# Kernel optimization log

Hardware: AMD Instinct MI355X
Metric: run time of the kernel (lower is better)

## Reference

```python
import jax, jax.numpy as jnp
import numpy as np

N = 50000          # nodes
E = 1_600_000      # edges (avg degree 32)
IN_N, IN_E = 16, 1 # fc_encoder hardwired input dims
H = 128            # per-layer out_node/out_edge channels (out//2 = 64 inner)
BN_EPS = 1e-5


def setup_inputs() -> dict:
    key = jax.random.key(0)
    ks = jax.random.split(key, 32)
    d = {}
    d["x"] = jax.random.normal(ks[0], (N, IN_N), jnp.float32)
    d["edge_attr"] = jax.random.normal(ks[1], (E, IN_E), jnp.float32)
    d["edge_index"] = jax.random.randint(ks[2], (2, E), 0, N)
    i = 3
    for l, (ni, ei) in enumerate([(IN_N, IN_E), (H, H)]):
        s_n = 1.0 / np.sqrt(ni)
        s_e = 1.0 / np.sqrt(ei)
        s_h = 1.0 / np.sqrt(H)
        d[f"l{l}_Wn"] = jax.random.normal(ks[i], (H // 2, ni), jnp.float32) * s_n; i += 1
        d[f"l{l}_We"] = jax.random.normal(ks[i], (H // 2, ei), jnp.float32) * s_e; i += 1
        d[f"l{l}_Wfn"] = jax.random.normal(ks[i], (H, H), jnp.float32) * s_h; i += 1
        d[f"l{l}_bfn"] = jax.random.normal(ks[i], (H,), jnp.float32) * s_h; i += 1
        d[f"l{l}_Wfe"] = jax.random.normal(ks[i], (H, H), jnp.float32) * s_h; i += 1
        d[f"l{l}_bfe"] = jax.random.normal(ks[i], (H,), jnp.float32) * s_h; i += 1
        d[f"l{l}_g"] = jax.random.uniform(ks[i], (H,), jnp.float32, 0.5, 1.5); i += 1
        d[f"l{l}_b"] = jax.random.normal(ks[i], (H,), jnp.float32) * 0.1; i += 1
        d[f"l{l}_rm"] = jax.random.normal(ks[i], (H,), jnp.float32) * 0.1; i += 1
        d[f"l{l}_rv"] = jax.random.uniform(ks[i], (H,), jnp.float32, 0.5, 1.5); i += 1
    return d


def _layer(x, ea, src, dst, Wn, We, Wfn, bfn, Wfe, bfe, g, b, rm, rv):
    # NodeEdgeInteraction_node (eval mode: dropout = identity)
    n1 = jax.nn.relu(x @ Wn.T)            # [N, H/2]
    e1 = jax.nn.relu(ea @ We.T)           # [E, H/2]
    # edge_updater: cat([n1[src] + n1[dst], e1])
    e2 = jnp.concatenate([n1[src] + n1[dst], e1], axis=-1)      # [E, H]
    # propagate: message = e1, sum-aggregate at destination (edge_index[1])
    agg = jax.ops.segment_sum(e1, dst, num_segments=x.shape[0])  # [N, H/2]
    n2 = jnp.concatenate([agg, n1], axis=-1)                     # [N, H]
    n2 = jax.nn.relu(n2 @ Wfn.T + bfn)
    e2 = jax.nn.relu(e2 @ Wfe.T + bfe)
    # BatchNorm1d (eval: running stats)
    n2 = (n2 - rm) * jax.lax.rsqrt(rv + BN_EPS) * g + b
    return n2, e2


def reference(x, edge_attr, edge_index,
              l0_Wn, l0_We, l0_Wfn, l0_bfn, l0_Wfe, l0_bfe, l0_g, l0_b, l0_rm, l0_rv,
              l1_Wn, l1_We, l1_Wfn, l1_bfn, l1_Wfe, l1_bfe, l1_g, l1_b, l1_rm, l1_rv):
    src, dst = edge_index[0], edge_index[1]
    x, edge_attr = _layer(x, edge_attr, src, dst,
                          l0_Wn, l0_We, l0_Wfn, l0_bfn, l0_Wfe, l0_bfe,
                          l0_g, l0_b, l0_rm, l0_rv)
    x, edge_attr = _layer(x, edge_attr, src, dst,
                          l1_Wn, l1_We, l1_Wfn, l1_bfn, l1_Wfe, l1_bfe,
                          l1_g, l1_b, l1_rm, l1_rv)
    return x  # GNNEncoder returns node embeddings only
```

## Files before the change

kernel.cpp:

```cpp
#include <hip/hip_runtime.h>

typedef unsigned short u16;
typedef __attribute__((ext_vector_type(8))) short short8;
typedef __attribute__((ext_vector_type(4))) float floatx4;

#define NN 50000
#define NE 1600000
#define BN_EPS 1e-5f
#define TPB 8

#define LDS_BARRIER() asm volatile("s_waitcnt lgkmcnt(0)\n\ts_barrier" ::: "memory")

__device__ __forceinline__ float bfu(u16 u) {
    union { unsigned u32; float f; } v; v.u32 = ((unsigned)u) << 16; return v.f;
}
__device__ __forceinline__ u16 f2bf(float f) {
    union { float f; unsigned u; } v; v.f = f;
    unsigned r = v.u + 0x7FFFu + ((v.u >> 16) & 1u);
    return (u16)(r >> 16);
}
__device__ __forceinline__ float ldf(const void* p, int i, int m) {
    return m ? ((const float*)p)[i] : bfu(((const u16*)p)[i]);
}

__global__ __launch_bounds__(256) void k_cvtw(const u16* __restrict__ x,
                                              const void* __restrict__ W0, const void* __restrict__ W1,
                                              const void* __restrict__ W2, const void* __restrict__ W3,
                                              const void* __restrict__ W4,
                                              const void* __restrict__ We0raw,
                                              u16* __restrict__ dst, float* __restrict__ PN,
                                              int* __restrict__ mode) {
    int t = threadIdx.x;
    __shared__ float sred[4];
    float mx = 0.f;
    for (int i = t; i < 4096; i += 256) mx = fmaxf(mx, fabsf(bfu(x[i])));
#pragma unroll
    for (int o = 32; o > 0; o >>= 1) mx = fmaxf(mx, __shfl_down(mx, o));
    if ((t & 63) == 0) sred[t >> 6] = mx;
    __syncthreads();
    float m2 = fmaxf(fmaxf(sred[0], sred[1]), fmaxf(sred[2], sred[3]));
    int m = (m2 > 1e4f) ? 1 : 0;
    if (blockIdx.x == 0 && t == 0) mode[0] = m;
    if (blockIdx.x == 256) {
        if (t < 128) {
            float p = 0.f, n = 0.f;
            for (int k = 0; k < 64; k++) {
                float w = ldf(We0raw, k, m);
                float wf = ldf(W0, t * 128 + 64 + k, m);
                p += fmaxf(w, 0.f) * wf;
                n += fminf(w, 0.f) * wf;
            }
            PN[t] = p; PN[128 + t] = n;
        }
        return;
    }
    int i = blockIdx.x * 256 + t;
    const void* src; int off;
    if (i < 16384)      { src = W0; off = i; }
    else if (i < 24576) { src = W1; off = i - 16384; }
    else if (i < 40960) { src = W2; off = i - 24576; }
    else if (i < 49152) { src = W3; off = i - 40960; }
    else                { src = W4; off = i - 49152; }
    dst[i] = m ? f2bf(((const float*)src)[off]) : ((const u16*)src)[off];
}

__global__ __launch_bounds__(256) void k_enc0h(const void* __restrict__ x, const void* __restrict__ Wn,
                                               u16* __restrict__ n1, const int* __restrict__ ei,
                                               const void* __restrict__ ea,
                                               float* __restrict__ sp, float* __restrict__ sn,
                                               const int* __restrict__ mf) {
    int b = blockIdx.x;
    int t = threadIdx.x;
    int m = mf[0];
    if (b >= 3125) {
        int e = (b - 3125) * 256 + t;
        float a = ldf(ea, e, m);
        int d = ei[NE + e];
        if (a > 0.f) atomicAdd(sp + d, a);
        else if (a < 0.f) atomicAdd(sn + d, a);
        return;
    }
    __shared__ float Wns[64 * 17];
    __shared__ float xsh[16][17];
    int n0 = b * 16;
    for (int i = t; i < 1024; i += 256) Wns[(i >> 4) * 17 + (i & 15)] = ldf(Wn, i, m);
    xsh[t >> 4][t & 15] = ldf(x, n0 * 16 + t, m);
    __syncthreads();
    int c = t & 63, ng = t >> 6;
    float a0 = 0.f, a1 = 0.f, a2 = 0.f, a3 = 0.f;
#pragma unroll
    for (int k = 0; k < 16; k++) {
        float wv = Wns[c * 17 + k];
        a0 += xsh[ng * 4 + 0][k] * wv;
        a1 += xsh[ng * 4 + 1][k] * wv;
        a2 += xsh[ng * 4 + 2][k] * wv;
        a3 += xsh[ng * 4 + 3][k] * wv;
    }
    n1[(n0 + ng * 4 + 0) * 64 + c] = f2bf(fmaxf(a0, 0.f));
    n1[(n0 + ng * 4 + 1) * 64 + c] = f2bf(fmaxf(a1, 0.f));
    n1[(n0 + ng * 4 + 2) * 64 + c] = f2bf(fmaxf(a2, 0.f));
    n1[(n0 + ng * 4 + 3) * 64 + c] = f2bf(fmaxf(a3, 0.f));
}

__global__ __launch_bounds__(256) void k_z(const u16* __restrict__ n1l0, const u16* __restrict__ Wfe0c,
                                           const void* __restrict__ bfe0, u16* __restrict__ z,
                                           const int* __restrict__ mf) {
    int m = mf[0];
    __shared__ __align__(16) u16 fs[64][72];
    int t = threadIdx.x;
    int n0 = blockIdx.x * 64;
    {
        int col = t & 63, rb = t >> 6;
#pragma unroll
        for (int i = 0; i < 16; i++) {
            int row = rb * 16 + i;
            int n = n0 + row;
            fs[row][col] = (n < NN) ? n1l0[n * 64 + col] : (u16)0;
        }
    }
    __syncthreads();
    int lane = t & 63, w = t >> 6, q = lane >> 4, nidx = lane & 15;
    const u16* ar = &fs[w * 16 + nidx][0];
    short8 a0 = *(const short8*)&ar[q * 8];
    short8 a1 = *(const short8*)&ar[32 + q * 8];
#pragma unroll
    for (int jt = 0; jt < 8; jt++) {
        int j = jt * 16 + nidx;
        const u16* wr = Wfe0c + j * 128;
        floatx4 acc = {0.f, 0.f, 0.f, 0.f};
        acc = __builtin_amdgcn_mfma_f32_16x16x32_bf16(a0, *(const short8*)&wr[q * 8], acc, 0, 0, 0);
        acc = __builtin_amdgcn_mfma_f32_16x16x32_bf16(a1, *(const short8*)&wr[32 + q * 8], acc, 0, 0, 0);
        float hb = 0.5f * ldf(bfe0, j, m);
#pragma unroll
        for (int r = 0; r < 4; r++) {
            int row = w * 16 + q * 4 + r;
            int n = n0 + row;
            if (n < NN) z[(size_t)n * 128 + j] = f2bf(acc[r] + hb);
        }
    }
}

__global__ __launch_bounds__(256) void k_node_l0(
    const u16* __restrict__ n1l0, const float* __restrict__ sp, const float* __restrict__ sn,
    const void* __restrict__ We0, const u16* __restrict__ Wfn0c, const void* __restrict__ bfn0,
    const void* __restrict__ g0, const void* __restrict__ b0,
    const void* __restrict__ rm0, const void* __restrict__ rv0,
    const u16* __restrict__ Wn1c, u16* __restrict__ n1l1, const int* __restrict__ mf) {
    int m = mf[0];
    __shared__ __align__(16) u16 fs[64][136];
    __shared__ __align__(16) u16 xs[64][136];
    int t = threadIdx.x;
    int n0 = blockIdx.x * 64;
    {
        int col = t & 127;
        int rbase = t >> 7;
        float wp = 0.f, wn = 0.f;
        if (col < 64) { float w0 = ldf(We0, col, m); wp = fmaxf(w0, 0.f); wn = fminf(w0, 0.f); }
#pragma unroll
        for (int i = 0; i < 32; i++) {
            int row = rbase + 2 * i;
            int n = n0 + row;
            float v = 0.f;
            if (n < NN) v = (col < 64) ? (wp * sp[n] + wn * sn[n]) : bfu(n1l0[n * 64 + col - 64]);
            fs[row][col] = f2bf(v);
        }
    }
    __syncthreads();
    int lane = t & 63, w = t >> 6, q = lane >> 4, nidx = lane & 15;
    {
        const u16* ar = &fs[w * 16 + nidx][0];
        short8 a0 = *(const short8*)&ar[q * 8];
        short8 a1 = *(const short8*)&ar[32 + q * 8];
        short8 a2 = *(const short8*)&ar[64 + q * 8];
        short8 a3 = *(const short8*)&ar[96 + q * 8];
#pragma unroll
        for (int jt = 0; jt < 8; jt++) {
            int j = jt * 16 + nidx;
            const u16* wr = Wfn0c + j * 128;
            floatx4 acc = {0.f, 0.f, 0.f, 0.f};
            acc = __builtin_amdgcn_mfma_f32_16x16x32_bf16(a0, *(const short8*)&wr[q * 8], acc, 0, 0, 0);
            acc = __builtin_amdgcn_mfma_f32_16x16x32_bf16(a1, *(const short8*)&wr[32 + q * 8], acc, 0, 0, 0);
            acc = __builtin_amdgcn_mfma_f32_16x16x32_bf16(a2, *(const short8*)&wr[64 + q * 8], acc, 0, 0, 0);
            acc = __builtin_amdgcn_mfma_f32_16x16x32_bf16(a3, *(const short8*)&wr[96 + q * 8], acc, 0, 0, 0);
            float bias = ldf(bfn0, j, m);
            float sc = ldf(g0, j, m) * rsqrtf(ldf(rv0, j, m) + BN_EPS);
            float sh = ldf(b0, j, m) - ldf(rm0, j, m) * sc;
#pragma unroll
            for (int r = 0; r < 4; r++) {
                int row = w * 16 + q * 4 + r;
                xs[row][j] = f2bf(fmaxf(acc[r] + bias, 0.f) * sc + sh);
            }
        }
    }
    __syncthreads();
    {
        const u16* ar = &xs[w * 16 + nidx][0];
        short8 a0 = *(const short8*)&ar[q * 8];
        short8 a1 = *(const short8*)&ar[32 + q * 8];
        short8 a2 = *(const short8*)&ar[64 + q * 8];
        short8 a3 = *(const short8*)&ar[96 + q * 8];
#pragma unroll
        for (int jt = 0; jt < 4; jt++) {
            int j = jt * 16 + nidx;
            const u16* wr = Wn1c + j * 128;
            floatx4 acc = {0.f, 0.f, 0.f, 0.f};
            acc = __builtin_amdgcn_mfma_f32_16x16x32_bf16(a0, *(const short8*)&wr[q * 8], acc, 0, 0, 0);
            acc = __builtin_amdgcn_mfma_f32_16x16x32_bf16(a1, *(const short8*)&wr[32 + q * 8], acc, 0, 0, 0);
            acc = __builtin_amdgcn_mfma_f32_16x16x32_bf16(a2, *(const short8*)&wr[64 + q * 8], acc, 0, 0, 0);
            acc = __builtin_amdgcn_mfma_f32_16x16x32_bf16(a3, *(const short8*)&wr[96 + q * 8], acc, 0, 0, 0);
#pragma unroll
            for (int r = 0; r < 4; r++) {
                int row = w * 16 + q * 4 + r;
                int n = n0 + row;
                if (n < NN) n1l1[n * 64 + j] = f2bf(fmaxf(acc[r], 0.f));
            }
        }
    }
}

__global__ __launch_bounds__(256) void k_edge9(
    const int* __restrict__ ei, const void* __restrict__ ea, const u16* __restrict__ z,
    const float* __restrict__ PN, const u16* __restrict__ We1c,
    float* __restrict__ agg, const int* __restrict__ mf) {
    int m = mf[0];
    __shared__ __align__(16) u16 h1s[2][16][136];
    int t = threadIdx.x;
    int lane = t & 63, w = t >> 6, q = lane >> 4, nidx = lane & 15;
    int ko = w * 32 + q * 8;
    float Pk[8], Nk[8];
#pragma unroll
    for (int j = 0; j < 8; j++) { Pk[j] = PN[ko + j]; Nk[j] = PN[128 + ko + j]; }
    int c2 = w * 16 + nidx;
    const u16* wr2 = We1c + c2 * 128;
    short8 wB0 = *(const short8*)&wr2[q * 8];
    short8 wB1 = *(const short8*)&wr2[32 + q * 8];
    short8 wB2 = *(const short8*)&wr2[64 + q * 8];
    short8 wB3 = *(const short8*)&wr2[96 + q * 8];

    int e0 = blockIdx.x * (16 * TPB);
    unsigned pk[TPB];
    float av[TPB];
#pragma unroll
    for (int tl = 0; tl < TPB; tl++) {
        int en = e0 + tl * 16 + nidx;
        unsigned s = (unsigned)ei[en];
        unsigned d = (unsigned)ei[NE + en];
        pk[tl] = s | (d << 16);
        av[tl] = ldf(ea, en, m);
    }
    short8 zsb[2], zdb[2];
#pragma unroll
    for (int tl = 0; tl < 2; tl++) {
        unsigned s = pk[tl] & 0xFFFFu, d = pk[tl] >> 16;
        zsb[tl] = *(const short8*)&z[(size_t)s * 128 + ko];
        zdb[tl] = *(const short8*)&z[(size_t)d * 128 + ko];
    }

#pragma unroll
    for (int tile = 0; tile < TPB; tile++) {
        short8 czs = zsb[tile & 1], czd = zdb[tile & 1];
        if (tile + 2 < TPB) {
            unsigned s = pk[tile + 2] & 0xFFFFu, d = pk[tile + 2] >> 16;
            zsb[tile & 1] = *(const short8*)&z[(size_t)s * 128 + ko];
            zdb[tile & 1] = *(const short8*)&z[(size_t)d * 128 + ko];
        }
        float cura = av[tile];
        float pf = fmaxf(cura, 0.f), nf = fminf(cura, 0.f);
        short8 hp;
#pragma unroll
        for (int j = 0; j < 8; j++) {
            float v = bfu((u16)czs[j]) + bfu((u16)czd[j]) + pf * Pk[j] + nf * Nk[j];
            hp[j] = (short)f2bf(fmaxf(v, 0.f));
        }
        *(short8*)&h1s[tile & 1][nidx][ko] = hp;
        LDS_BARRIER();
        const u16* arow = &h1s[tile & 1][nidx][0];
        floatx4 accA = {0.f, 0.f, 0.f, 0.f};
        floatx4 accB = {0.f, 0.f, 0.f, 0.f};
        accA = __builtin_amdgcn_mfma_f32_16x16x32_bf16(*(const short8*)&arow[q * 8], wB0, accA, 0, 0, 0);
        accB = __builtin_amdgcn_mfma_f32_16x16x32_bf16(*(const short8*)&arow[32 + q * 8], wB1, accB, 0, 0, 0);
        accA = __builtin_amdgcn_mfma_f32_16x16x32_bf16(*(const short8*)&arow[64 + q * 8], wB2, accA, 0, 0, 0);
        accB = __builtin_amdgcn_mfma_f32_16x16x32_bf16(*(const short8*)&arow[96 + q * 8], wB3, accB, 0, 0, 0);
        int pkt = (int)pk[tile];
        unsigned x0 = (unsigned)__shfl(pkt, q * 4 + 0);
        unsigned x1 = (unsigned)__shfl(pkt, q * 4 + 1);
        unsigned x2 = (unsigned)__shfl(pkt, q * 4 + 2);
        unsigned x3 = (unsigned)__shfl(pkt, q * 4 + 3);
        atomicAdd(agg + (size_t)(x0 >> 16) * 64 + c2, fmaxf(accA[0] + accB[0], 0.f));
        atomicAdd(agg + (size_t)(x1 >> 16) * 64 + c2, fmaxf(accA[1] + accB[1], 0.f));
        atomicAdd(agg + (size_t)(x2 >> 16) * 64 + c2, fmaxf(accA[2] + accB[2], 0.f));
        atomicAdd(agg + (size_t)(x3 >> 16) * 64 + c2, fmaxf(accA[3] + accB[3], 0.f));
    }
}

__global__ __launch_bounds__(256) void k_node_l1(
    const u16* __restrict__ n1l1, const float* __restrict__ agg,
    const u16* __restrict__ Wfn1c, const void* __restrict__ bfn1,
    const void* __restrict__ g1, const void* __restrict__ b1,
    const void* __restrict__ rm1, const void* __restrict__ rv1,
    void* __restrict__ out, const int* __restrict__ mf) {
    int m = mf[0];
    __shared__ __align__(16) u16 fs[64][136];
    int t = threadIdx.x;
    int n0 = blockIdx.x * 64;
    {
        int col = t & 127;
        int rbase = t >> 7;
#pragma unroll
        for (int i = 0; i < 32; i++) {
            int row = rbase + 2 * i;
            int n = n0 + row;
            float v = 0.f;
            if (n < NN) v = (col < 64) ? agg[n * 64 + col] : bfu(n1l1[n * 64 + col - 64]);
            fs[row][col] = f2bf(v);
        }
    }
    __syncthreads();
    int lane = t & 63, w = t >> 6, q = lane >> 4, nidx = lane & 15;
    const u16* ar = &fs[w * 16 + nidx][0];
    short8 a0 = *(const short8*)&ar[q * 8];
    short8 a1 = *(const short8*)&ar[32 + q * 8];
    short8 a2 = *(const short8*)&ar[64 + q * 8];
    short8 a3 = *(const short8*)&ar[96 + q * 8];
#pragma unroll
    for (int jt = 0; jt < 8; jt++) {
        int j = jt * 16 + nidx;
        const u16* wr = Wfn1c + j * 128;
        floatx4 acc = {0.f, 0.f, 0.f, 0.f};
        acc = __builtin_amdgcn_mfma_f32_16x16x32_bf16(a0, *(const short8*)&wr[q * 8], acc, 0, 0, 0);
        acc = __builtin_amdgcn_mfma_f32_16x16x32_bf16(a1, *(const short8*)&wr[32 + q * 8], acc, 0, 0, 0);
        acc = __builtin_amdgcn_mfma_f32_16x16x32_bf16(a2, *(const short8*)&wr[64 + q * 8], acc, 0, 0, 0);
        acc = __builtin_amdgcn_mfma_f32_16x16x32_bf16(a3, *(const short8*)&wr[96 + q * 8], acc, 0, 0, 0);
        float bias = ldf(bfn1, j, m);
        float sc = ldf(g1, j, m) * rsqrtf(ldf(rv1, j, m) + BN_EPS);
        float sh = ldf(b1, j, m) - ldf(rm1, j, m) * sc;
#pragma unroll
        for (int r = 0; r < 4; r++) {
            int row = w * 16 + q * 4 + r;
            int n = n0 + row;
            if (n < NN) {
                float v = fmaxf(acc[r] + bias, 0.f) * sc + sh;
                if (m) ((float*)out)[n * 128 + j] = v;
                else   ((u16*)out)[n * 128 + j] = f2bf(v);
            }
        }
    }
}

extern "C" void kernel_launch(void* const* d_in, const int* in_sizes, int n_in,
                              void* d_out, int out_size, void* d_ws, size_t ws_size,
                              hipStream_t stream) {
    const void* x    = d_in[0];
    const void* ea   = d_in[1];
    const int*  ei   = (const int*)d_in[2];
    const void* Wn0  = d_in[3];
    const void* We0  = d_in[4];
    const void* Wfn0 = d_in[5];
    const void* bfn0 = d_in[6];
    const void* Wfe0 = d_in[7];
    const void* bfe0 = d_in[8];
    const void* g0   = d_in[9];
    const void* b0   = d_in[10];
    const void* rm0  = d_in[11];
    const void* rv0  = d_in[12];
    const void* Wn1  = d_in[13];
    const void* We1  = d_in[14];
    const void* Wfn1 = d_in[15];
    const void* bfn1 = d_in[16];
    const void* g1   = d_in[19];
    const void* b1   = d_in[20];
    const void* rm1  = d_in[21];
    const void* rv1  = d_in[22];

    float* wsf    = (float*)d_ws;
    float* agg    = wsf;
    u16*   n1l0   = (u16*)(wsf + 3200000);
    u16*   n1l1   = (u16*)(wsf + 4800000);
    float* sp     = wsf + 6400000;
    float* sn     = wsf + 6450000;
    float* PN     = wsf + 6500000;
    u16*   Wc     = (u16*)(wsf + 6500256);
    int*   mode   = (int*)(wsf + 6533024);
    u16*   z      = (u16*)(wsf + 6533028);
    u16* Wfe0c = Wc;
    u16* We1c  = Wc + 16384;
    u16* Wfn0c = Wc + 24576;
    u16* Wn1c  = Wc + 40960;
    u16* Wfn1c = Wc + 49152;

    hipMemsetAsync(sp, 0, 100000 * sizeof(float), stream);
    hipMemsetAsync(agg, 0, 3200000 * sizeof(float), stream);

    k_cvtw<<<257, 256, 0, stream>>>((const u16*)x, Wfe0, We1, Wfn0, Wn1, Wfn1,
                                    We0, Wc, PN, mode);
    k_enc0h<<<9375, 256, 0, stream>>>(x, Wn0, n1l0, ei, ea, sp, sn, mode);
    k_z<<<782, 256, 0, stream>>>(n1l0, Wfe0c, bfe0, z, mode);
    k_node_l0<<<782, 256, 0, stream>>>(n1l0, sp, sn, We0, Wfn0c, bfn0,
                                       g0, b0, rm0, rv0, Wn1c, n1l1, mode);
    k_edge9<<<NE / (16 * TPB), 256, 0, stream>>>(ei, ea, z, PN, We1c, agg, mode);
    k_node_l1<<<782, 256, 0, stream>>>(n1l1, agg, Wfn1c, bfn1,
                                       g1, b1, rm1, rv1, d_out, mode);
}
```

Measured before the change: 620.1 us.

## Sort edges by destination and combine atomics per run in edge kernel

Adds a counting sort of edges by destination: per-node counts, a three-kernel prefix scan, and a scatter that writes packed src/dst pairs and edge attributes into a scratch area in the output buffer. The edge kernel then reads the sorted edges and accumulates consecutive same-destination rows in registers, issuing one atomic per run instead of one per edge. This targets the cost of float atomics into agg. In exchange it adds four small kernels, an atomic-based scatter that reads and writes 1.6M edges, and the output buffer is reused as temporary storage before the final kernel writes it.

```diff
diff --git a/kernel.cpp b/kernel.cpp
--- a/kernel.cpp
+++ b/kernel.cpp
@@ -7,6 +7,7 @@
 #define NN 50000
 #define NE 1600000
 #define BN_EPS 1e-5f
+#define NSCAN 196
 #define TPB 8
 
 #define LDS_BARRIER() asm volatile("s_waitcnt lgkmcnt(0)\n\ts_barrier" ::: "memory")
@@ -68,7 +69,7 @@
                                                u16* __restrict__ n1, const int* __restrict__ ei,
                                                const void* __restrict__ ea,
                                                float* __restrict__ sp, float* __restrict__ sn,
-                                               const int* __restrict__ mf) {
+                                               int* __restrict__ cnt, const int* __restrict__ mf) {
     int b = blockIdx.x;
     int t = threadIdx.x;
     int m = mf[0];
@@ -76,6 +77,7 @@
         int e = (b - 3125) * 256 + t;
         float a = ldf(ea, e, m);
         int d = ei[NE + e];
+        atomicAdd(cnt + d, 1);
         if (a > 0.f) atomicAdd(sp + d, a);
         else if (a < 0.f) atomicAdd(sn + d, a);
         return;
@@ -100,6 +102,64 @@
     n1[(n0 + ng * 4 + 1) * 64 + c] = f2bf(fmaxf(a1, 0.f));
     n1[(n0 + ng * 4 + 2) * 64 + c] = f2bf(fmaxf(a2, 0.f));
     n1[(n0 + ng * 4 + 3) * 64 + c] = f2bf(fmaxf(a3, 0.f));
+}
+
+__global__ __launch_bounds__(256) void k_scan1(const int* __restrict__ cnt, int* __restrict__ bsum) {
+    int t = threadIdx.x;
+    int idx = blockIdx.x * 256 + t;
+    int v = (idx < NN) ? cnt[idx] : 0;
+#pragma unroll
+    for (int o = 32; o > 0; o >>= 1) v += __shfl_down(v, o);
+    __shared__ int s[4];
+    if ((t & 63) == 0) s[t >> 6] = v;
+    __syncthreads();
+    if (t == 0) bsum[blockIdx.x] = s[0] + s[1] + s[2] + s[3];
+}
+
+__global__ __launch_bounds__(256) void k_scan2(int* __restrict__ bsum) {
+    __shared__ int sh[256];
+    int t = threadIdx.x;
+    int v = (t < NSCAN) ? bsum[t] : 0;
+    sh[t] = v;
+    __syncthreads();
+    for (int o = 1; o < 256; o <<= 1) {
+        int u = (t >= o) ? sh[t - o] : 0;
+        __syncthreads();
+        sh[t] += u;
+        __syncthreads();
+    }
+    if (t < NSCAN) bsum[t] = sh[t] - v;
+}
+
+__global__ __launch_bounds__(256) void k_scan3(const int* __restrict__ cnt, const int* __restrict__ bsum,
+                                               int* __restrict__ cursor) {
+    __shared__ int sh[256];
+    int t = threadIdx.x;
+    int idx = blockIdx.x * 256 + t;
+    int v = (idx < NN) ? cnt[idx] : 0;
+    sh[t] = v;
+    __syncthreads();
+    for (int o = 1; o < 256; o <<= 1) {
+        int u = (t >= o) ? sh[t - o] : 0;
+        __syncthreads();
+        sh[t] += u;
+        __syncthreads();
+    }
+    int excl = sh[t] - v + bsum[blockIdx.x];
+    if (idx < NN) cursor[idx] = excl;
+}
+
+__global__ __launch_bounds__(256) void k_scatter(const void* __restrict__ ea, const int* __restrict__ ei,
+                                                 int* __restrict__ cursor, int* __restrict__ packed4,
+                                                 float* __restrict__ eaf, const int* __restrict__ mf) {
+    int m = mf[0];
+    int e = blockIdx.x * 256 + threadIdx.x;
+    int d = ei[NE + e];
+    int s = ei[e];
+    float a = ldf(ea, e, m);
+    int p = atomicAdd(cursor + d, 1);
+    packed4[p] = s | (d << 16);
+    eaf[p] = a;
 }
 
 __global__ __launch_bounds__(256) void k_z(const u16* __restrict__ n1l0, const u16* __restrict__ Wfe0c,
@@ -218,11 +278,10 @@
     }
 }
 
-__global__ __launch_bounds__(256) void k_edge9(
-    const int* __restrict__ ei, const void* __restrict__ ea, const u16* __restrict__ z,
+__global__ __launch_bounds__(256) void k_edge13(
+    const int* __restrict__ packed4, const float* __restrict__ eaf, const u16* __restrict__ z,
     const float* __restrict__ PN, const u16* __restrict__ We1c,
-    float* __restrict__ agg, const int* __restrict__ mf) {
-    int m = mf[0];
+    float* __restrict__ agg) {
     __shared__ __align__(16) u16 h1s[2][16][136];
     int t = threadIdx.x;
     int lane = t & 63, w = t >> 6, q = lane >> 4, nidx = lane & 15;
@@ -243,10 +302,8 @@
 #pragma unroll
     for (int tl = 0; tl < TPB; tl++) {
         int en = e0 + tl * 16 + nidx;
-        unsigned s = (unsigned)ei[en];
-        unsigned d = (unsigned)ei[NE + en];
-        pk[tl] = s | (d << 16);
-        av[tl] = ldf(ea, en, m);
+        pk[tl] = (unsigned)packed4[en];
+        av[tl] = eaf[en];
     }
     short8 zsb[2], zdb[2];
 #pragma unroll
@@ -255,6 +312,9 @@
         zsb[tl] = *(const short8*)&z[(size_t)s * 128 + ko];
         zdb[tl] = *(const short8*)&z[(size_t)d * 128 + ko];
     }
+
+    unsigned cur = ((unsigned)__shfl((int)pk[0], q * 4)) >> 16;
+    float run = 0.f;
 
 #pragma unroll
     for (int tile = 0; tile < TPB; tile++) {
@@ -282,15 +342,19 @@
         accA = __builtin_amdgcn_mfma_f32_16x16x32_bf16(*(const short8*)&arow[64 + q * 8], wB2, accA, 0, 0, 0);
         accB = __builtin_amdgcn_mfma_f32_16x16x32_bf16(*(const short8*)&arow[96 + q * 8], wB3, accB, 0, 0, 0);
         int pkt = (int)pk[tile];
-        unsigned x0 = (unsigned)__shfl(pkt, q * 4 + 0);
-        unsigned x1 = (unsigned)__shfl(pkt, q * 4 + 1);
-        unsigned x2 = (unsigned)__shfl(pkt, q * 4 + 2);
-        unsigned x3 = (unsigned)__shfl(pkt, q * 4 + 3);
-        atomicAdd(agg + (size_t)(x0 >> 16) * 64 + c2, fmaxf(accA[0] + accB[0], 0.f));
-        atomicAdd(agg + (size_t)(x1 >> 16) * 64 + c2, fmaxf(accA[1] + accB[1], 0.f));
-        atomicAdd(agg + (size_t)(x2 >> 16) * 64 + c2, fmaxf(accA[2] + accB[2], 0.f));
-        atomicAdd(agg + (size_t)(x3 >> 16) * 64 + c2, fmaxf(accA[3] + accB[3], 0.f));
-    }
+#pragma unroll
+        for (int r = 0; r < 4; r++) {
+            unsigned d = ((unsigned)__shfl(pkt, q * 4 + r)) >> 16;
+            float v = fmaxf(accA[r] + accB[r], 0.f);
+            if (d == cur) {
+                run += v;
+            } else {
+                atomicAdd(agg + (size_t)cur * 64 + c2, run);
+                cur = d; run = v;
+            }
+        }
+    }
+    atomicAdd(agg + (size_t)cur * 64 + c2, run);
 }
 
 __global__ __launch_bounds__(256) void k_node_l1(
@@ -378,26 +442,35 @@
     u16*   n1l1   = (u16*)(wsf + 4800000);
     float* sp     = wsf + 6400000;
     float* sn     = wsf + 6450000;
-    float* PN     = wsf + 6500000;
-    u16*   Wc     = (u16*)(wsf + 6500256);
-    int*   mode   = (int*)(wsf + 6533024);
-    u16*   z      = (u16*)(wsf + 6533028);
+    int*   cnt    = (int*)(wsf + 6500000);
+    int*   cursor = (int*)(wsf + 6550000);
+    int*   bsum   = (int*)(wsf + 6600000);
+    float* PN     = wsf + 6600256;
+    u16*   Wc     = (u16*)(wsf + 6600512);
+    int*   mode   = (int*)(wsf + 6633280);
+    u16*   z      = (u16*)(wsf + 6633284);
     u16* Wfe0c = Wc;
     u16* We1c  = Wc + 16384;
     u16* Wfn0c = Wc + 24576;
     u16* Wn1c  = Wc + 40960;
     u16* Wfn1c = Wc + 49152;
-
-    hipMemsetAsync(sp, 0, 100000 * sizeof(float), stream);
+    int*   packed4 = (int*)d_out;
+    float* eaf     = (float*)((char*)d_out + 6400000);
+
+    hipMemsetAsync(sp, 0, 150000 * sizeof(float), stream);
     hipMemsetAsync(agg, 0, 3200000 * sizeof(float), stream);
 
     k_cvtw<<<257, 256, 0, stream>>>((const u16*)x, Wfe0, We1, Wfn0, Wn1, Wfn1,
                                     We0, Wc, PN, mode);
-    k_enc0h<<<9375, 256, 0, stream>>>(x, Wn0, n1l0, ei, ea, sp, sn, mode);
+    k_enc0h<<<9375, 256, 0, stream>>>(x, Wn0, n1l0, ei, ea, sp, sn, cnt, mode);
+    k_scan1<<<NSCAN, 256, 0, stream>>>(cnt, bsum);
+    k_scan2<<<1, 256, 0, stream>>>(bsum);
+    k_scan3<<<NSCAN, 256, 0, stream>>>(cnt, bsum, cursor);
+    k_scatter<<<6250, 256, 0, stream>>>(ea, ei, cursor, packed4, eaf, mode);
     k_z<<<782, 256, 0, stream>>>(n1l0, Wfe0c, bfe0, z, mode);
     k_node_l0<<<782, 256, 0, stream>>>(n1l0, sp, sn, We0, Wfn0c, bfn0,
                                        g0, b0, rm0, rv0, Wn1c, n1l1, mode);
-    k_edge9<<<NE / (16 * TPB), 256, 0, stream>>>(ei, ea, z, PN, We1c, agg, mode);
+    k_edge13<<<NE / (16 * TPB), 256, 0, stream>>>(packed4, eaf, z, PN, We1c, agg);
     k_node_l1<<<782, 256, 0, stream>>>(n1l1, agg, Wfn1c, bfn1,
                                        g1, b1, rm1, rv1, d_out, mode);
 }
```

After: 632.7 us. 1.02x slower.

## Bucket edges by destination and accumulate edge messages in LDS windows

Applied to the files above, without the earlier changes.

Counts edges per 16-node destination bucket, scans the counts, and scatters packed (src,dst,attr) records into bucket order in the output buffer. The layer-1 edge kernel then reads these sorted records and accumulates messages for a 48-node destination window in shared memory. It flushes to global memory only once per block, replacing per-edge global float atomics. This adds a counting pass, a serial scan and a scatter pass with contended counter atomics, plus an extra edge-record write and read.

```diff
diff --git a/kernel.cpp b/kernel.cpp
--- a/kernel.cpp
+++ b/kernel.cpp
@@ -7,7 +7,9 @@
 #define NN 50000
 #define NE 1600000
 #define BN_EPS 1e-5f
+#define NB 3125
 #define TPB 8
+#define WIN 48
 
 #define LDS_BARRIER() asm volatile("s_waitcnt lgkmcnt(0)\n\ts_barrier" ::: "memory")
 
@@ -68,7 +70,7 @@
                                                u16* __restrict__ n1, const int* __restrict__ ei,
                                                const void* __restrict__ ea,
                                                float* __restrict__ sp, float* __restrict__ sn,
-                                               const int* __restrict__ mf) {
+                                               int* __restrict__ bcnt, const int* __restrict__ mf) {
     int b = blockIdx.x;
     int t = threadIdx.x;
     int m = mf[0];
@@ -76,6 +78,7 @@
         int e = (b - 3125) * 256 + t;
         float a = ldf(ea, e, m);
         int d = ei[NE + e];
+        atomicAdd(bcnt + (d >> 4), 1);
         if (a > 0.f) atomicAdd(sp + d, a);
         else if (a < 0.f) atomicAdd(sn + d, a);
         return;
@@ -100,6 +103,46 @@
     n1[(n0 + ng * 4 + 1) * 64 + c] = f2bf(fmaxf(a1, 0.f));
     n1[(n0 + ng * 4 + 2) * 64 + c] = f2bf(fmaxf(a2, 0.f));
     n1[(n0 + ng * 4 + 3) * 64 + c] = f2bf(fmaxf(a3, 0.f));
+}
+
+__global__ __launch_bounds__(256) void k_bscan(const int* __restrict__ bcnt, int* __restrict__ bcur) {
+    __shared__ int sh[256];
+    __shared__ int carry;
+    int t = threadIdx.x;
+    if (t == 0) carry = 0;
+    __syncthreads();
+    for (int base = 0; base < NB; base += 256) {
+        int idx = base + t;
+        int v = (idx < NB) ? bcnt[idx] : 0;
+        sh[t] = v;
+        __syncthreads();
+        for (int o = 1; o < 256; o <<= 1) {
+            int u = (t >= o) ? sh[t - o] : 0;
+            __syncthreads();
+            sh[t] += u;
+            __syncthreads();
+        }
+        int excl = sh[t] - v + carry;
+        if (idx < NB) bcur[idx] = excl;
+        __syncthreads();
+        if (t == 255) carry += sh[255];
+        __syncthreads();
+    }
+}
+
+__global__ __launch_bounds__(256) void k_scatter(const void* __restrict__ ea, const int* __restrict__ ei,
+                                                 int* __restrict__ bcur, int2* __restrict__ edata,
+                                                 const int* __restrict__ mf) {
+    int m = mf[0];
+    int e = blockIdx.x * 256 + threadIdx.x;
+    int d = ei[NE + e];
+    int s = ei[e];
+    float a = ldf(ea, e, m);
+    int p = atomicAdd(bcur + (d >> 4), 1);
+    int2 v;
+    v.x = s | (d << 16);
+    v.y = __float_as_int(a);
+    edata[p] = v;
 }
 
 __global__ __launch_bounds__(256) void k_z(const u16* __restrict__ n1l0, const u16* __restrict__ Wfe0c,
@@ -218,12 +261,12 @@
     }
 }
 
-__global__ __launch_bounds__(256) void k_edge9(
-    const int* __restrict__ ei, const void* __restrict__ ea, const u16* __restrict__ z,
+__global__ __launch_bounds__(256) void k_edge15(
+    const int2* __restrict__ edata, const u16* __restrict__ z,
     const float* __restrict__ PN, const u16* __restrict__ We1c,
-    float* __restrict__ agg, const int* __restrict__ mf) {
-    int m = mf[0];
+    float* __restrict__ agg) {
     __shared__ __align__(16) u16 h1s[2][16][136];
+    __shared__ float accs[WIN][65];
     int t = threadIdx.x;
     int lane = t & 63, w = t >> 6, q = lane >> 4, nidx = lane & 15;
     int ko = w * 32 + q * 8;
@@ -237,17 +280,18 @@
     short8 wB2 = *(const short8*)&wr2[64 + q * 8];
     short8 wB3 = *(const short8*)&wr2[96 + q * 8];
 
+    for (int i = t; i < WIN * 65; i += 256) ((float*)accs)[i] = 0.f;
+
     int e0 = blockIdx.x * (16 * TPB);
     unsigned pk[TPB];
     float av[TPB];
 #pragma unroll
     for (int tl = 0; tl < TPB; tl++) {
-        int en = e0 + tl * 16 + nidx;
-        unsigned s = (unsigned)ei[en];
-        unsigned d = (unsigned)ei[NE + en];
-        pk[tl] = s | (d << 16);
-        av[tl] = ldf(ea, en, m);
-    }
+        int2 ed = edata[e0 + tl * 16 + nidx];
+        pk[tl] = (unsigned)ed.x;
+        av[tl] = __int_as_float(ed.y);
+    }
+    unsigned dbase = ((((unsigned)__shfl((int)pk[0], 0)) >> 16) >> 4) << 4;
     short8 zsb[2], zdb[2];
 #pragma unroll
     for (int tl = 0; tl < 2; tl++) {
@@ -282,14 +326,21 @@
         accA = __builtin_amdgcn_mfma_f32_16x16x32_bf16(*(const short8*)&arow[64 + q * 8], wB2, accA, 0, 0, 0);
         accB = __builtin_amdgcn_mfma_f32_16x16x32_bf16(*(const short8*)&arow[96 + q * 8], wB3, accB, 0, 0, 0);
         int pkt = (int)pk[tile];
-        unsigned x0 = (unsigned)__shfl(pkt, q * 4 + 0);
-        unsigned x1 = (unsigned)__shfl(pkt, q * 4 + 1);
-        unsigned x2 = (unsigned)__shfl(pkt, q * 4 + 2);
-        unsigned x3 = (unsigned)__shfl(pkt, q * 4 + 3);
-        atomicAdd(agg + (size_t)(x0 >> 16) * 64 + c2, fmaxf(accA[0] + accB[0], 0.f));
-        atomicAdd(agg + (size_t)(x1 >> 16) * 64 + c2, fmaxf(accA[1] + accB[1], 0.f));
-        atomicAdd(agg + (size_t)(x2 >> 16) * 64 + c2, fmaxf(accA[2] + accB[2], 0.f));
-        atomicAdd(agg + (size_t)(x3 >> 16) * 64 + c2, fmaxf(accA[3] + accB[3], 0.f));
+#pragma unroll
+        for (int r = 0; r < 4; r++) {
+            unsigned d = ((unsigned)__shfl(pkt, q * 4 + r)) >> 16;
+            unsigned dl = d - dbase;
+            float v = fmaxf(accA[r] + accB[r], 0.f);
+            if (dl < WIN) atomicAdd(&accs[dl][c2], v);
+            else          atomicAdd(agg + (size_t)d * 64 + c2, v);
+        }
+    }
+    LDS_BARRIER();
+    for (int i = t; i < WIN * 64; i += 256) {
+        int dl = i >> 6, c = i & 63;
+        float v = accs[dl][c];
+        unsigned n = dbase + dl;
+        if (v != 0.f && n < NN) atomicAdd(agg + (size_t)n * 64 + c, v);
     }
 }
 
@@ -378,26 +429,31 @@
     u16*   n1l1   = (u16*)(wsf + 4800000);
     float* sp     = wsf + 6400000;
     float* sn     = wsf + 6450000;
-    float* PN     = wsf + 6500000;
-    u16*   Wc     = (u16*)(wsf + 6500256);
-    int*   mode   = (int*)(wsf + 6533024);
-    u16*   z      = (u16*)(wsf + 6533028);
+    int*   bcnt   = (int*)(wsf + 6500000);
+    int*   bcur   = (int*)(wsf + 6503125);
+    float* PN     = wsf + 6506250;
+    u16*   Wc     = (u16*)(wsf + 6506506);
+    int*   mode   = (int*)(wsf + 6539274);
+    u16*   z      = (u16*)(wsf + 6539278);
     u16* Wfe0c = Wc;
     u16* We1c  = Wc + 16384;
     u16* Wfn0c = Wc + 24576;
     u16* Wn1c  = Wc + 40960;
     u16* Wfn1c = Wc + 49152;
-
-    hipMemsetAsync(sp, 0, 100000 * sizeof(float), stream);
+    int2* edata = (int2*)d_out;
+
+    hipMemsetAsync(sp, 0, 103125 * sizeof(float), stream);
     hipMemsetAsync(agg, 0, 3200000 * sizeof(float), stream);
 
     k_cvtw<<<257, 256, 0, stream>>>((const u16*)x, Wfe0, We1, Wfn0, Wn1, Wfn1,
                                     We0, Wc, PN, mode);
-    k_enc0h<<<9375, 256, 0, stream>>>(x, Wn0, n1l0, ei, ea, sp, sn, mode);
+    k_enc0h<<<9375, 256, 0, stream>>>(x, Wn0, n1l0, ei, ea, sp, sn, bcnt, mode);
+    k_bscan<<<1, 256, 0, stream>>>(bcnt, bcur);
+    k_scatter<<<6250, 256, 0, stream>>>(ea, ei, bcur, edata, mode);
     k_z<<<782, 256, 0, stream>>>(n1l0, Wfe0c, bfe0, z, mode);
     k_node_l0<<<782, 256, 0, stream>>>(n1l0, sp, sn, We0, Wfn0c, bfn0,
                                        g0, b0, rm0, rv0, Wn1c, n1l1, mode);
-    k_edge9<<<NE / (16 * TPB), 256, 0, stream>>>(ei, ea, z, PN, We1c, agg, mode);
+    k_edge15<<<NE / (16 * TPB), 256, 0, stream>>>(edata, z, PN, We1c, agg);
     k_node_l1<<<782, 256, 0, stream>>>(n1l1, agg, Wfn1c, bfn1,
                                        g1, b1, rm1, rv1, d_out, mode);
 }
```

After: 1.142 ms. +84.1%, slower.
